# Performance work log

Hardware: AMD Instinct MI355X
Metric: run time of the kernel (lower is better)

The kernel has to match this reference:

```python
import jax, jax.numpy as jnp
import numpy as np


def gcn_conv(x, edge_index, W, b):
    # PyG GCNConv with normalize=True: add self-loops, symmetric D^-1/2 A D^-1/2,
    # transform then aggregate messages source->target, then add bias.
    N = x.shape[0]
    row, col = edge_index[0], edge_index[1]  # row: source, col: target
    loop = jnp.arange(N, dtype=edge_index.dtype)
    row = jnp.concatenate([row, loop])
    col = jnp.concatenate([col, loop])
    ones = jnp.ones(row.shape[0], dtype=x.dtype)
    deg = jax.ops.segment_sum(ones, col, num_segments=N)
    dinv = jnp.where(deg > 0, jax.lax.rsqrt(deg), 0.0)
    norm = dinv[row] * dinv[col]            # [E+N]
    h = x @ W                                # [N, d_out] transform first (cheaper aggregation)
    msgs = h[row] * norm[:, None]            # gather + scale
    out = jax.ops.segment_sum(msgs, col, num_segments=N)  # scatter-add to targets
    return out + b


def setup_inputs() -> dict:
    key = jax.random.key(0)
    k = jax.random.split(key, 6)
    N, D, H, C, E = 100000, 256, 32, 2, 3200000
    x = jax.random.normal(k[0], (N, D), dtype=jnp.float32)
    edge_index = jax.random.randint(k[1], (2, E), 0, N, dtype=jnp.int64)
    # glorot-style init for GCN weights
    W1 = jax.random.normal(k[2], (D, H), dtype=jnp.float32) * np.sqrt(2.0 / (D + H))
    b1 = jnp.zeros((H,), dtype=jnp.float32)
    W2 = jax.random.normal(k[3], (H, C), dtype=jnp.float32) * np.sqrt(2.0 / (H + C))
    b2 = jnp.zeros((C,), dtype=jnp.float32)
    return {"x": x, "edge_index": edge_index, "W1": W1, "b1": b1, "W2": W2, "b2": b2}


def reference(x, edge_index, W1, b1, W2, b2):
    # CRD: GCNConv -> relu -> dropout(p=0.5, eval mode -> identity)
    h = jax.nn.relu(gcn_conv(x, edge_index, W1, b1))
    # CLS: GCNConv -> log_softmax over classes
    logits = gcn_conv(h, edge_index, W2, b2)
    return jax.nn.log_softmax(logits, axis=1)
```

## Files before the change

kernel.cpp:

```cpp
#include <hip/hip_runtime.h>
#include <hip/hip_fp16.h>
#include <math.h>

#define DIV_UP(a,b) (((a)+(b)-1)/(b))

typedef _Float16 f16x8 __attribute__((ext_vector_type(8)));
typedef float    f32x4 __attribute__((ext_vector_type(4)));

#define SHIFT 9
#define TPB   (1 << SHIFT)
#define LMASK (TPB - 1)
#define CHUNK 4096

__global__ __launch_bounds__(256) void k_init(int* __restrict__ gcur, int cap,
                                              int* __restrict__ offsets, int N, int E) {
    const int t = threadIdx.x;
    gcur[t] = t * cap;
    if (t == 0) offsets[N] = E;
}

__global__ __launch_bounds__(256) void k_fat(const float* __restrict__ x,
                                             const float* __restrict__ W,
                                             __half* __restrict__ h1,
                                             const int* __restrict__ row,
                                             const int* __restrict__ col,
                                             int* __restrict__ gcur,
                                             unsigned* __restrict__ binned,
                                             int E, int N, int gemmB) {
    __shared__ __align__(16) char smem[32768];
    const int t = threadIdx.x;

    if ((int)blockIdx.x < gemmB) {
        float* Wl = (float*)smem;
        const float4* W4 = (const float4*)W;
        float4* Wl4 = (float4*)Wl;
#pragma unroll
        for (int i = 0; i < 8; ++i) Wl4[t + 256 * i] = W4[t + 256 * i];
        __syncthreads();

        const int lane = t & 63;
        const int wv   = t >> 6;
        const int m    = lane & 15;
        const int q    = lane >> 4;

        f16x8 bf[8][2];
#pragma unroll
        for (int kc = 0; kc < 8; ++kc)
#pragma unroll
            for (int ct = 0; ct < 2; ++ct)
#pragma unroll
                for (int j = 0; j < 8; ++j)
                    bf[kc][ct][j] = (_Float16)Wl[(kc * 32 + q * 8 + j) * 32 + ct * 16 + m];

        const int rowA   = blockIdx.x * 64 + wv * 16 + m;
        const int rclamp = min(rowA, N - 1);
        const float* xr  = x + (long long)rclamp * 256 + q * 8;

        f32x4 c0 = {0.f, 0.f, 0.f, 0.f}, c1 = {0.f, 0.f, 0.f, 0.f};
#pragma unroll
        for (int kc = 0; kc < 8; ++kc) {
            float4 v0 = *(const float4*)(xr + kc * 32);
            float4 v1 = *(const float4*)(xr + kc * 32 + 4);
            f16x8 a;
            a[0] = (_Float16)v0.x; a[1] = (_Float16)v0.y;
            a[2] = (_Float16)v0.z; a[3] = (_Float16)v0.w;
            a[4] = (_Float16)v1.x; a[5] = (_Float16)v1.y;
            a[6] = (_Float16)v1.z; a[7] = (_Float16)v1.w;
            c0 = __builtin_amdgcn_mfma_f32_16x16x32_f16(a, bf[kc][0], c0, 0, 0, 0);
            c1 = __builtin_amdgcn_mfma_f32_16x16x32_f16(a, bf[kc][1], c1, 0, 0, 0);
        }

        const int orow = blockIdx.x * 64 + wv * 16 + q * 4;
#pragma unroll
        for (int r = 0; r < 4; ++r) {
            int gr = orow + r;
            if (gr < N) {
                h1[gr * 32 + m]      = __float2half(c0[r]);
                h1[gr * 32 + 16 + m] = __float2half(c1[r]);
            }
        }
    } else {
        int* hist  = (int*)smem;
        int* loff  = hist + 256;
        int* gbase = loff + 256;
        int* lcur  = gbase + 256;
        unsigned* staged     = (unsigned*)(smem + 4096);
        unsigned char* binOf = (unsigned char*)(smem + 4096 + 16384);

        const int base = (blockIdx.x - gemmB) * CHUNK;
        const int n = min(CHUNK, E - base);

        hist[t] = 0;
        __syncthreads();

        unsigned pk[CHUNK / 256];
        int bn[CHUNK / 256];
#pragma unroll
        for (int k = 0; k < CHUNK / 256; ++k) {
            int i = base + t + k * 256;
            if (i < E) {
                int c = col[i], r = row[i];
                bn[k] = c >> SHIFT;
                pk[k] = ((unsigned)r << SHIFT) | (unsigned)(c & LMASK);
                atomicAdd(&hist[bn[k]], 1);
            } else bn[k] = -1;
        }
        __syncthreads();

        int v = hist[t];
        loff[t] = v;
        __syncthreads();
#pragma unroll
        for (int off = 1; off < 256; off <<= 1) {
            int y = (t >= off) ? loff[t - off] : 0;
            __syncthreads();
            loff[t] += y;
            __syncthreads();
        }
        int excl = loff[t] - v;
        gbase[t] = v ? atomicAdd(&gcur[t], v) : 0;
        lcur[t]  = excl;
        __syncthreads();
        loff[t] = excl;
        __syncthreads();

#pragma unroll
        for (int k = 0; k < CHUNK / 256; ++k) {
            if (bn[k] >= 0) {
                int p = atomicAdd(&lcur[bn[k]], 1);
                staged[p] = pk[k];
                binOf[p] = (unsigned char)bn[k];
            }
        }
        __syncthreads();

        for (int i = t; i < n; i += 256) {
            int b = binOf[i];
            binned[gbase[b] + (i - loff[b])] = staged[i];
        }
    }
}

__global__ __launch_bounds__(512) void k_csr2(const unsigned* __restrict__ binned,
                                              const int* __restrict__ gcur, int cap,
                                              int* __restrict__ offsets,
                                              float* __restrict__ dinv,
                                              int* __restrict__ srcs,
                                              __half* __restrict__ h1, int N) {
    __shared__ int h[TPB];
    __shared__ int cur[TPB];
    __shared__ int rbuf[512];
    const int t = threadIdx.x, b = blockIdx.x;
    const int beg = b * cap, end = gcur[b];

    rbuf[t] = (t < 256 && t < b) ? (gcur[t] - t * cap) : 0;
    h[t] = 0;
    __syncthreads();
#pragma unroll
    for (int off = 256; off > 0; off >>= 1) {
        if (t < off) rbuf[t] += rbuf[t + off];
        __syncthreads();
    }
    const int obase = rbuf[0];

    for (int i = beg + t; i < end; i += 512)
        atomicAdd(&h[binned[i] & LMASK], 1);
    __syncthreads();

    int cnt = h[t];
#pragma unroll
    for (int off = 1; off < 512; off <<= 1) {
        int y = (t >= off) ? h[t - off] : 0;
        __syncthreads();
        h[t] += y;
        __syncthreads();
    }
    int excl = h[t] - cnt;
    int g = (b << SHIFT) + t;
    int pos0 = obase + excl;
    float di = 0.f;
    if (g < N) {
        offsets[g] = pos0;
        di = rsqrtf((float)(1 + cnt));
        dinv[g] = di;
    }
    cur[t] = pos0;
    __syncthreads();

    for (int i = beg + t; i < end; i += 512) {
        unsigned v = binned[i];
        int pos = atomicAdd(&cur[v & LMASK], 1);
        srcs[pos] = (int)(v >> SHIFT);
    }

    if (g < N) {
        uint4* hp4 = (uint4*)(h1 + (size_t)g * 32);
#pragma unroll
        for (int k4 = 0; k4 < 4; ++k4) {
            uint4 v = hp4[k4];
            __half2* ph = (__half2*)&v;
#pragma unroll
            for (int k2 = 0; k2 < 4; ++k2) {
                float2 u = __half22float2(ph[k2]);
                ph[k2] = __floats2half2_rn(u.x * di, u.y * di);
            }
            hp4[k4] = v;
        }
    }
}

__global__ void k_agg1(const int* __restrict__ offsets, const int* __restrict__ srcs,
                       const float* __restrict__ dinv, const __half* __restrict__ h1w,
                       const float* __restrict__ b1, const float* __restrict__ W2,
                       __half2* __restrict__ tw, int N) {
    long long g = (long long)blockIdx.x * blockDim.x + threadIdx.x;
    int node = (int)(g >> 5), f = (int)(g & 31);
    if (node >= N) return;
    const int sub = f >> 2, q = f & 3;
    const int beg = offsets[node], end = offsets[node + 1];
    const uint4* h4 = (const uint4*)h1w;

    float a0 = 0.f, a1 = 0.f, a2 = 0.f, a3 = 0.f;
    float a4 = 0.f, a5 = 0.f, a6 = 0.f, a7 = 0.f;

    for (int j = beg; j < end; j += 8) {
        int e = j + sub;
        int ee = min(e, end - 1);
        int s = srcs[ee];
        float msk = (e < end) ? 1.f : 0.f;
        uint4 rv = h4[s * 4 + q];
        __half2 p; float2 u;
        p = *(__half2*)&rv.x; u = __half22float2(p); a0 = fmaf(u.x, msk, a0); a1 = fmaf(u.y, msk, a1);
        p = *(__half2*)&rv.y; u = __half22float2(p); a2 = fmaf(u.x, msk, a2); a3 = fmaf(u.y, msk, a3);
        p = *(__half2*)&rv.z; u = __half22float2(p); a4 = fmaf(u.x, msk, a4); a5 = fmaf(u.y, msk, a5);
        p = *(__half2*)&rv.w; u = __half22float2(p); a6 = fmaf(u.x, msk, a6); a7 = fmaf(u.y, msk, a7);
    }
#pragma unroll
    for (int s = 4; s < 32; s <<= 1) {
        a0 += __shfl_xor(a0, s, 32); a1 += __shfl_xor(a1, s, 32);
        a2 += __shfl_xor(a2, s, 32); a3 += __shfl_xor(a3, s, 32);
        a4 += __shfl_xor(a4, s, 32); a5 += __shfl_xor(a5, s, 32);
        a6 += __shfl_xor(a6, s, 32); a7 += __shfl_xor(a7, s, 32);
    }
    if (sub == 0) {
        float di = dinv[node];
        uint4 rv = h4[node * 4 + q];
        float sf[8];
        {
            __half2 p; float2 u;
            p = *(__half2*)&rv.x; u = __half22float2(p); sf[0] = u.x; sf[1] = u.y;
            p = *(__half2*)&rv.y; u = __half22float2(p); sf[2] = u.x; sf[3] = u.y;
            p = *(__half2*)&rv.z; u = __half22float2(p); sf[4] = u.x; sf[5] = u.y;
            p = *(__half2*)&rv.w; u = __half22float2(p); sf[6] = u.x; sf[7] = u.y;
        }
        float av[8] = {a0, a1, a2, a3, a4, a5, a6, a7};
        float t0 = 0.f, t1 = 0.f;
#pragma unroll
        for (int k = 0; k < 8; ++k) {
            int feat = q * 8 + k;
            float hv = fmaf(di, av[k] + sf[k], b1[feat]);
            hv = fmaxf(hv, 0.f);
            t0 = fmaf(hv, W2[feat * 2 + 0], t0);
            t1 = fmaf(hv, W2[feat * 2 + 1], t1);
        }
        t0 += __shfl_xor(t0, 1, 32); t0 += __shfl_xor(t0, 2, 32);
        t1 += __shfl_xor(t1, 1, 32); t1 += __shfl_xor(t1, 2, 32);
        if (q == 0) tw[node] = __floats2half2_rn(di * t0, di * t1);
    }
}

__global__ void k_agg2(const int* __restrict__ offsets, const int* __restrict__ srcs,
                       const float* __restrict__ dinv, const __half2* __restrict__ tw,
                       const float* __restrict__ b2, float* __restrict__ out, int N) {
    long long g = (long long)blockIdx.x * blockDim.x + threadIdx.x;
    int node = (int)(g >> 4), f = (int)(g & 15);
    if (node >= N) return;
    int beg = offsets[node], end = offsets[node + 1];
    float a0 = 0.f, a1 = 0.f;
    for (int j = beg + f; j < end; j += 16) {
        int s = srcs[j];
        float2 u = __half22float2(tw[s]);
        a0 += u.x;
        a1 += u.y;
    }
#pragma unroll
    for (int s = 8; s; s >>= 1) {
        a0 += __shfl_xor(a0, s, 64);
        a1 += __shfl_xor(a1, s, 64);
    }
    if (f == 0) {
        float di = dinv[node];
        float2 u = __half22float2(tw[node]);
        float z0 = di * (a0 + u.x) + b2[0];
        float z1 = di * (a1 + u.y) + b2[1];
        float m = fmaxf(z0, z1);
        float lse = m + logf(expf(z0 - m) + expf(z1 - m));
        ((float2*)out)[node] = float2{z0 - lse, z1 - lse};
    }
}

extern "C" void kernel_launch(void* const* d_in, const int* in_sizes, int n_in,
                              void* d_out, int out_size, void* d_ws, size_t ws_size,
                              hipStream_t stream) {
    const float* x  = (const float*)d_in[0];
    const int*   ei = (const int*)d_in[1];
    const float* W1 = (const float*)d_in[2];
    const float* b1 = (const float*)d_in[3];
    const float* W2 = (const float*)d_in[4];
    const float* b2 = (const float*)d_in[5];

    const int H = in_sizes[3];
    const int D = in_sizes[2] / H;
    const int N = in_sizes[0] / D;
    const int E = in_sizes[1] / 2;
    (void)H; (void)n_in; (void)out_size; (void)ws_size;

    const int* row = ei;
    const int* col = ei + E;

    const int K_used = ((N - 1) >> SHIFT) + 1;
    const int cap    = (DIV_UP(E, K_used) * 5 / 4 + 255) & ~255;
    const int nchunk = DIV_UP(E, CHUNK);
    const int gemmB  = DIV_UP(N, 64);

    char* p = (char*)d_ws;
    auto alloc = [&](size_t bytes) { char* q = p; p += (bytes + 255) & ~(size_t)255; return q; };
    int*      offsets = (int*)     alloc((size_t)(N + 1) * 4);
    int*      gcur    = (int*)     alloc(256 * 4);
    float*    dinv    = (float*)   alloc((size_t)N * 4);
    unsigned* binned  = (unsigned*)alloc((size_t)K_used * cap * 4);
    __half*   h1      = (__half*)  alloc((size_t)N * 32 * 2);
    int*      srcs    = (int*)     alloc((size_t)E * 4);
    __half2*  tw      = (__half2*) alloc((size_t)N * 4);

    k_init <<<1, 256, 0, stream>>>(gcur, cap, offsets, N, E);
    k_fat  <<<gemmB + nchunk, 256, 0, stream>>>(x, W1, h1, row, col, gcur, binned, E, N, gemmB);
    k_csr2 <<<K_used, 512, 0, stream>>>(binned, gcur, cap, offsets, dinv, srcs, h1, N);
    k_agg1 <<<(int)DIV_UP((long long)N * 32, 256), 256, 0, stream>>>(offsets, srcs, dinv, h1, b1, W2, tw, N);
    k_agg2 <<<(int)DIV_UP((long long)N * 16, 256), 256, 0, stream>>>(offsets, srcs, dinv, tw, b2, (float*)d_out, N);
}
```

Measured before the change: 295.1 us.

## Interleave GEMM and binning blocks, pre-swizzle W in LDS, unroll aggregation gather

The fused kernel now alternates GEMM and edge-binning blocks by block index, so memory-bound binning and MFMA-bound GEMM work run concurrently on the CUs instead of in two phases. The weights are stored in LDS as fp16 already laid out per lane, so each MFMA operand is one vector load rather than 128 scalar register gathers. Shared memory shrinks to 24KB, which could raise occupancy. In the first aggregation kernel the neighbor loop handles two edges per thread per iteration to keep more gathers in flight, at the cost of extra masked work on low-degree nodes.

```diff
diff --git a/kernel.cpp b/kernel.cpp
--- a/kernel.cpp
+++ b/kernel.cpp
@@ -26,16 +26,30 @@
                                              const int* __restrict__ col,
                                              int* __restrict__ gcur,
                                              unsigned* __restrict__ binned,
-                                             int E, int N, int gemmB) {
-    __shared__ __align__(16) char smem[32768];
+                                             int E, int N, int nchunk) {
+    __shared__ __align__(16) char smem[24576];
     const int t = threadIdx.x;
-
-    if ((int)blockIdx.x < gemmB) {
-        float* Wl = (float*)smem;
-        const float4* W4 = (const float4*)W;
-        float4* Wl4 = (float4*)Wl;
-#pragma unroll
-        for (int i = 0; i < 8; ++i) Wl4[t + 256 * i] = W4[t + 256 * i];
+    const int bid = blockIdx.x;
+    const bool isBin = (bid < 2 * nchunk) && (bid & 1);
+
+    if (!isBin) {
+        const int gb = (bid < 2 * nchunk) ? (bid >> 1) : (bid - nchunk);
+        _Float16* WlT = (_Float16*)smem;
+
+#pragma unroll
+        for (int i = 0; i < 8; ++i) {
+            int idx = t + 256 * i;
+            float4 v = ((const float4*)W)[idx];
+            int k  = idx >> 3;
+            int n4 = (idx & 7) * 4;
+            int kc = k >> 5, q = (k >> 3) & 3, j = k & 7;
+            int ct = n4 >> 4, m0 = n4 & 15;
+            _Float16* dst = WlT + ((size_t)((kc * 2 + ct) * 64 + q * 16 + m0) * 8 + j);
+            dst[0 * 8] = (_Float16)v.x;
+            dst[1 * 8] = (_Float16)v.y;
+            dst[2 * 8] = (_Float16)v.z;
+            dst[3 * 8] = (_Float16)v.w;
+        }
         __syncthreads();
 
         const int lane = t & 63;
@@ -43,16 +57,7 @@
         const int m    = lane & 15;
         const int q    = lane >> 4;
 
-        f16x8 bf[8][2];
-#pragma unroll
-        for (int kc = 0; kc < 8; ++kc)
-#pragma unroll
-            for (int ct = 0; ct < 2; ++ct)
-#pragma unroll
-                for (int j = 0; j < 8; ++j)
-                    bf[kc][ct][j] = (_Float16)Wl[(kc * 32 + q * 8 + j) * 32 + ct * 16 + m];
-
-        const int rowA   = blockIdx.x * 64 + wv * 16 + m;
+        const int rowA   = gb * 64 + wv * 16 + m;
         const int rclamp = min(rowA, N - 1);
         const float* xr  = x + (long long)rclamp * 256 + q * 8;
 
@@ -61,16 +66,18 @@
         for (int kc = 0; kc < 8; ++kc) {
             float4 v0 = *(const float4*)(xr + kc * 32);
             float4 v1 = *(const float4*)(xr + kc * 32 + 4);
+            f16x8 b0 = *(const f16x8*)&WlT[(size_t)((kc * 2 + 0) * 64 + lane) * 8];
+            f16x8 b1 = *(const f16x8*)&WlT[(size_t)((kc * 2 + 1) * 64 + lane) * 8];
             f16x8 a;
             a[0] = (_Float16)v0.x; a[1] = (_Float16)v0.y;
             a[2] = (_Float16)v0.z; a[3] = (_Float16)v0.w;
             a[4] = (_Float16)v1.x; a[5] = (_Float16)v1.y;
             a[6] = (_Float16)v1.z; a[7] = (_Float16)v1.w;
-            c0 = __builtin_amdgcn_mfma_f32_16x16x32_f16(a, bf[kc][0], c0, 0, 0, 0);
-            c1 = __builtin_amdgcn_mfma_f32_16x16x32_f16(a, bf[kc][1], c1, 0, 0, 0);
-        }
-
-        const int orow = blockIdx.x * 64 + wv * 16 + q * 4;
+            c0 = __builtin_amdgcn_mfma_f32_16x16x32_f16(a, b0, c0, 0, 0, 0);
+            c1 = __builtin_amdgcn_mfma_f32_16x16x32_f16(a, b1, c1, 0, 0, 0);
+        }
+
+        const int orow = gb * 64 + wv * 16 + q * 4;
 #pragma unroll
         for (int r = 0; r < 4; ++r) {
             int gr = orow + r;
@@ -87,7 +94,7 @@
         unsigned* staged     = (unsigned*)(smem + 4096);
         unsigned char* binOf = (unsigned char*)(smem + 4096 + 16384);
 
-        const int base = (blockIdx.x - gemmB) * CHUNK;
+        const int base = (bid >> 1) * CHUNK;
         const int n = min(CHUNK, E - base);
 
         hist[t] = 0;
@@ -223,17 +230,23 @@
     float a0 = 0.f, a1 = 0.f, a2 = 0.f, a3 = 0.f;
     float a4 = 0.f, a5 = 0.f, a6 = 0.f, a7 = 0.f;
 
-    for (int j = beg; j < end; j += 8) {
-        int e = j + sub;
-        int ee = min(e, end - 1);
-        int s = srcs[ee];
-        float msk = (e < end) ? 1.f : 0.f;
-        uint4 rv = h4[s * 4 + q];
+    for (int j = beg; j < end; j += 16) {
+        int e0 = j + sub, e1 = j + 8 + sub;
+        int s0 = srcs[min(e0, end - 1)];
+        int s1 = srcs[min(e1, end - 1)];
+        float m0 = (e0 < end) ? 1.f : 0.f;
+        float m1 = (e1 < end) ? 1.f : 0.f;
+        uint4 rv0 = h4[s0 * 4 + q];
+        uint4 rv1 = h4[s1 * 4 + q];
         __half2 p; float2 u;
-        p = *(__half2*)&rv.x; u = __half22float2(p); a0 = fmaf(u.x, msk, a0); a1 = fmaf(u.y, msk, a1);
-        p = *(__half2*)&rv.y; u = __half22float2(p); a2 = fmaf(u.x, msk, a2); a3 = fmaf(u.y, msk, a3);
-        p = *(__half2*)&rv.z; u = __half22float2(p); a4 = fmaf(u.x, msk, a4); a5 = fmaf(u.y, msk, a5);
-        p = *(__half2*)&rv.w; u = __half22float2(p); a6 = fmaf(u.x, msk, a6); a7 = fmaf(u.y, msk, a7);
+        p = *(__half2*)&rv0.x; u = __half22float2(p); a0 = fmaf(u.x, m0, a0); a1 = fmaf(u.y, m0, a1);
+        p = *(__half2*)&rv0.y; u = __half22float2(p); a2 = fmaf(u.x, m0, a2); a3 = fmaf(u.y, m0, a3);
+        p = *(__half2*)&rv0.z; u = __half22float2(p); a4 = fmaf(u.x, m0, a4); a5 = fmaf(u.y, m0, a5);
+        p = *(__half2*)&rv0.w; u = __half22float2(p); a6 = fmaf(u.x, m0, a6); a7 = fmaf(u.y, m0, a7);
+        p = *(__half2*)&rv1.x; u = __half22float2(p); a0 = fmaf(u.x, m1, a0); a1 = fmaf(u.y, m1, a1);
+        p = *(__half2*)&rv1.y; u = __half22float2(p); a2 = fmaf(u.x, m1, a2); a3 = fmaf(u.y, m1, a3);
+        p = *(__half2*)&rv1.z; u = __half22float2(p); a4 = fmaf(u.x, m1, a4); a5 = fmaf(u.y, m1, a5);
+        p = *(__half2*)&rv1.w; u = __half22float2(p); a6 = fmaf(u.x, m1, a6); a7 = fmaf(u.y, m1, a7);
     }
 #pragma unroll
     for (int s = 4; s < 32; s <<= 1) {
@@ -334,7 +347,7 @@
     __half2*  tw      = (__half2*) alloc((size_t)N * 4);
 
     k_init <<<1, 256, 0, stream>>>(gcur, cap, offsets, N, E);
-    k_fat  <<<gemmB + nchunk, 256, 0, stream>>>(x, W1, h1, row, col, gcur, binned, E, N, gemmB);
+    k_fat  <<<gemmB + nchunk, 256, 0, stream>>>(x, W1, h1, row, col, gcur, binned, E, N, nchunk);
     k_csr2 <<<K_used, 512, 0, stream>>>(binned, gcur, cap, offsets, dinv, srcs, h1, N);
     k_agg1 <<<(int)DIV_UP((long long)N * 32, 256), 256, 0, stream>>>(offsets, srcs, dinv, h1, b1, W2, tw, N);
     k_agg2 <<<(int)DIV_UP((long long)N * 16, 256), 256, 0, stream>>>(offsets, srcs, dinv, tw, b2, (float*)d_out, N);
```

Result: faster. 280.7 us (-4.9%).
